# Performance work log

Measured on AMD Instinct MI355X. Metric: run time of the kernel, lower is better.

Reference implementation:

```python
import jax, jax.numpy as jnp
import numpy as np

B, T, C, H = 2, 2048, 1024, 16
D = C // H  # head_dim = 64
CH = C // 2


def _ln(x, g, b, eps=1e-5):
    m = x.mean(-1, keepdims=True)
    v = ((x - m) ** 2).mean(-1, keepdims=True)
    return (x - m) / jnp.sqrt(v + eps) * g + b


def setup_inputs() -> dict:
    key = jax.random.key(0)
    ks = iter(jax.random.split(key, 32))
    w = lambda shp: jax.random.normal(next(ks), shp, dtype=jnp.float32) * 0.02
    inp = {
        'x': jax.random.normal(next(ks), (B, T, C), dtype=jnp.float32),
        'attention_mask': jnp.ones((B, T, T), dtype=jnp.int32),
        # importance_net: Linear(C,C/2), LN(C/2), GELU, Linear(C/2,1), Sigmoid
        'imp_w1': w((C, CH)), 'imp_b1': jnp.zeros((CH,)),
        'imp_g': jnp.ones((CH,)), 'imp_beta': jnp.zeros((CH,)),
        'imp_w2': w((CH, 1)), 'imp_b2': jnp.zeros((1,)),
        # reasoning_net: Linear(C,C), LN(C), GELU, Linear(C,C)
        'rsn_w1': w((C, C)), 'rsn_b1': jnp.zeros((C,)),
        'rsn_g': jnp.ones((C,)), 'rsn_beta': jnp.zeros((C,)),
        'rsn_w2': w((C, C)), 'rsn_b2': jnp.zeros((C,)),
        # attention projections
        'q_w': w((C, C)), 'q_b': jnp.zeros((C,)),
        'k_w': w((C, C)), 'k_b': jnp.zeros((C,)),
        'v_w': w((C, C)), 'v_b': jnp.zeros((C,)),
        'o_w': w((C, C)), 'o_b': jnp.zeros((C,)),
        # temp_net: Linear(C,C/2), LN(C/2), GELU, Linear(C/2,H)
        'tmp_w1': w((C, CH)), 'tmp_b1': jnp.zeros((CH,)),
        'tmp_g': jnp.ones((CH,)), 'tmp_beta': jnp.zeros((CH,)),
        'tmp_w2': w((CH, H)), 'tmp_b2': jnp.zeros((H,)),
        # output LayerNorm
        'norm_g': jnp.ones((C,)), 'norm_b': jnp.zeros((C,)),
    }
    return inp


def reference(x, attention_mask, imp_w1, imp_b1, imp_g, imp_beta, imp_w2, imp_b2,
              rsn_w1, rsn_b1, rsn_g, rsn_beta, rsn_w2, rsn_b2,
              q_w, q_b, k_w, k_b, v_w, v_b, o_w, o_b,
              tmp_w1, tmp_b1, tmp_g, tmp_beta, tmp_w2, tmp_b2,
              norm_g, norm_b):
    Bz, Tz, Cz = x.shape
    # importance gating: [B,T,1]
    h = jax.nn.gelu(_ln(x @ imp_w1 + imp_b1, imp_g, imp_beta), approximate=False)
    importance = jnp.maximum(jax.nn.sigmoid(h @ imp_w2 + imp_b2), 1e-6)
    xi = x * importance
    # reasoning net on gated input
    h = jax.nn.gelu(_ln(xi @ rsn_w1 + rsn_b1, rsn_g, rsn_beta), approximate=False)
    reasoned = h @ rsn_w2 + rsn_b2
    # projections
    q = (reasoned @ q_w + q_b).reshape(Bz, Tz, H, D).transpose(0, 2, 1, 3)
    k = (xi @ k_w + k_b).reshape(Bz, Tz, H, D).transpose(0, 2, 1, 3)
    v = (x @ v_w + v_b).reshape(Bz, Tz, H, D).transpose(0, 2, 1, 3)
    # per-(batch,head) temperature
    ht = jax.nn.gelu(_ln(reasoned.mean(axis=1) @ tmp_w1 + tmp_b1, tmp_g, tmp_beta), approximate=False)
    temp = jax.nn.softplus(ht @ tmp_w2 + tmp_b2) + 0.5  # [B,H]
    # attention with mask and learned temperature before softmax
    scale = 1.0 / jnp.sqrt(jnp.float32(D))
    attn = jnp.einsum('bhqd,bhkd->bhqk', q, k) * scale
    attn = jnp.where(attention_mask[:, None] == 0, -jnp.inf, attn)
    attn = attn * temp[:, :, None, None]
    attn = jax.nn.softmax(attn, axis=-1)
    # dropout is identity in eval mode
    out = jnp.einsum('bhqk,bhkd->bhqd', attn, v)
    out = out.transpose(0, 2, 1, 3).reshape(Bz, Tz, Cz)
    out = out @ o_w + o_b
    return _ln(x + out, norm_g, norm_b)
```

## Files before the change

kernel.cpp:

```cpp
#include <hip/hip_runtime.h>
#include <hip/hip_bf16.h>
#include <math.h>

#define BB 2
#define TT 2048
#define CC 1024
#define HH 16
#define DD 64
#define CHALF 512
#define NN (BB * TT)

typedef __attribute__((ext_vector_type(8))) short short8;
typedef __attribute__((ext_vector_type(4))) short short4_t;
typedef __attribute__((ext_vector_type(4))) float f32x4;

__device__ __forceinline__ float gelu_exact(float x) {
    return 0.5f * x * (1.0f + erff(x * 0.70710678118654752f));
}

__device__ __forceinline__ short f2bf(float f) {
    __hip_bfloat16 h = __float2bfloat16(f);
    short s;
    __builtin_memcpy(&s, &h, 2);
    return s;
}

__device__ __forceinline__ void async_copy16(const void* g, void* l) {
    __builtin_amdgcn_global_load_lds(
        (const __attribute__((address_space(1))) void*)g,
        (__attribute__((address_space(3))) void*)l, 16, 0, 0);
}

__global__ __launch_bounds__(256) void conv_bf16(
    const float* __restrict__ X, __hip_bfloat16* __restrict__ O) {
    int i = (blockIdx.x * 256 + threadIdx.x) * 8;
    float4 a = *(const float4*)&X[i];
    float4 b = *(const float4*)&X[i + 4];
    __hip_bfloat16 o[8] = {
        __float2bfloat16(a.x), __float2bfloat16(a.y),
        __float2bfloat16(a.z), __float2bfloat16(a.w),
        __float2bfloat16(b.x), __float2bfloat16(b.y),
        __float2bfloat16(b.z), __float2bfloat16(b.w)};
    *(float4*)&O[i] = *(float4*)o;
}

__global__ __launch_bounds__(256) void conv_transpose_all(
    const float* w0, const float* w1, const float* w2, const float* w3,
    const float* w4, const float* w5, const float* w6,
    __hip_bfloat16* t0, __hip_bfloat16* t1, __hip_bfloat16* t2,
    __hip_bfloat16* t3, __hip_bfloat16* t4, __hip_bfloat16* t5,
    __hip_bfloat16* t6) {
    const float* W;
    __hip_bfloat16* Wt;
    int N = 1024;
    switch (blockIdx.z) {
        case 0: W = w0; Wt = t0; N = 512; break;
        case 1: W = w1; Wt = t1; break;
        case 2: W = w2; Wt = t2; break;
        case 3: W = w3; Wt = t3; break;
        case 4: W = w4; Wt = t4; break;
        case 5: W = w5; Wt = t5; break;
        default: W = w6; Wt = t6; break;
    }
    int n0 = blockIdx.x * 64, k0 = blockIdx.y * 64;
    if (n0 >= N) return;
    __shared__ float T[64][65];
    int tid = threadIdx.x;
    int c = tid & 63, r4 = tid >> 6;
#pragma unroll
    for (int i = 0; i < 16; ++i) {
        int row = i * 4 + r4;
        T[row][c] = W[(size_t)(k0 + row) * N + n0 + c];
    }
    __syncthreads();
#pragma unroll
    for (int i = 0; i < 16; ++i) {
        int row = i * 4 + r4;
        Wt[(size_t)(n0 + row) * CC + k0 + c] = __float2bfloat16(T[c][row]);
    }
}

template <bool BF16OUT>
__global__ __launch_bounds__(256) void gemm_mfma64(
    const short* __restrict__ A, const short* __restrict__ Wt,
    const float* __restrict__ bias, float* __restrict__ Cf,
    __hip_bfloat16* __restrict__ Cb, int M, int N, int K) {
    __shared__ short As[64][32];
    __shared__ short Bs[128][32];
    int tid = threadIdx.x;
    int wave = tid >> 6, lane = tid & 63;
    int m16 = lane & 15, quad = lane >> 4;
    int wm = wave >> 1, wn = wave & 1;
    int row0 = blockIdx.y * 64, col0 = blockIdx.x * 128;
    int lr = lane >> 2;
    int kof = (lane & 3) * 8;

    f32x4 acc[2][4];
#pragma unroll
    for (int i = 0; i < 2; ++i)
#pragma unroll
        for (int j = 0; j < 4; ++j) acc[i][j] = (f32x4){0.f, 0.f, 0.f, 0.f};

    for (int k0 = 0; k0 < K; k0 += 32) {
        async_copy16(A + (size_t)(row0 + wave * 16 + lr) * K + k0 + kof,
                     &As[wave * 16][0]);
#pragma unroll
        for (int j = 0; j < 2; ++j) {
            int rbase = wave * 32 + j * 16;
            async_copy16(Wt + (size_t)(col0 + rbase + lr) * K + k0 + kof,
                         &Bs[rbase][0]);
        }
        __syncthreads();
        short8 af[2], bfr[4];
#pragma unroll
        for (int i = 0; i < 2; ++i)
            af[i] = *(const short8*)&As[wm * 32 + i * 16 + m16][quad * 8];
#pragma unroll
        for (int j = 0; j < 4; ++j)
            bfr[j] = *(const short8*)&Bs[wn * 64 + j * 16 + m16][quad * 8];
#pragma unroll
        for (int i = 0; i < 2; ++i)
#pragma unroll
            for (int j = 0; j < 4; ++j)
                acc[i][j] = __builtin_amdgcn_mfma_f32_16x16x32_bf16(
                    af[i], bfr[j], acc[i][j], 0, 0, 0);
        __syncthreads();
    }
#pragma unroll
    for (int i = 0; i < 2; ++i) {
#pragma unroll
        for (int j = 0; j < 4; ++j) {
            int col = col0 + wn * 64 + j * 16 + m16;
            float bv = bias[col];
#pragma unroll
            for (int rr = 0; rr < 4; ++rr) {
                int row = row0 + wm * 32 + i * 16 + quad * 4 + rr;
                float val = acc[i][j][rr] + bv;
                if (BF16OUT)
                    Cb[(size_t)row * N + col] = __float2bfloat16(val);
                else
                    Cf[(size_t)row * N + col] = val;
            }
        }
    }
}

__global__ __launch_bounds__(256) void gemm_qkv(
    const short* __restrict__ Aq, const short* __restrict__ Ak,
    const short* __restrict__ Av, const short* __restrict__ Wq,
    const short* __restrict__ Wk, const short* __restrict__ Wv,
    const float* __restrict__ bq, const float* __restrict__ bk,
    const float* __restrict__ bv, __hip_bfloat16* __restrict__ Cq,
    __hip_bfloat16* __restrict__ Ck, __hip_bfloat16* __restrict__ Cv,
    const float* __restrict__ tmp) {
    int z = blockIdx.z;
    const short* A = (z == 0) ? Aq : (z == 1) ? Ak : Av;
    const short* Wt = (z == 0) ? Wq : (z == 1) ? Wk : Wv;
    const float* bias = (z == 0) ? bq : (z == 1) ? bk : bv;
    __hip_bfloat16* C = (z == 0) ? Cq : (z == 1) ? Ck : Cv;

    __shared__ short As[128][32];
    __shared__ short Bs[128][32];
    int tid = threadIdx.x;
    int wave = tid >> 6, lane = tid & 63;
    int m16 = lane & 15, quad = lane >> 4;
    int wm = wave >> 1, wn = wave & 1;
    int row0 = blockIdx.y * 128, col0 = blockIdx.x * 128;
    int lr = lane >> 2;
    int kof = (lane & 3) * 8;

    float scale = 1.0f;
    if (z == 0) scale = tmp[(row0 >> 11) * HH + (col0 >> 6) + wn] * 0.125f;

    f32x4 acc[4][4];
#pragma unroll
    for (int i = 0; i < 4; ++i)
#pragma unroll
        for (int j = 0; j < 4; ++j) acc[i][j] = (f32x4){0.f, 0.f, 0.f, 0.f};

    for (int k0 = 0; k0 < CC; k0 += 32) {
#pragma unroll
        for (int j = 0; j < 2; ++j) {
            int rbase = wave * 32 + j * 16;
            async_copy16(A + (size_t)(row0 + rbase + lr) * CC + k0 + kof,
                         &As[rbase][0]);
            async_copy16(Wt + (size_t)(col0 + rbase + lr) * CC + k0 + kof,
                         &Bs[rbase][0]);
        }
        __syncthreads();
        short8 af[4], bfr[4];
#pragma unroll
        for (int i = 0; i < 4; ++i)
            af[i] = *(const short8*)&As[wm * 64 + i * 16 + m16][quad * 8];
#pragma unroll
        for (int j = 0; j < 4; ++j)
            bfr[j] = *(const short8*)&Bs[wn * 64 + j * 16 + m16][quad * 8];
#pragma unroll
        for (int i = 0; i < 4; ++i)
#pragma unroll
            for (int j = 0; j < 4; ++j)
                acc[i][j] = __builtin_amdgcn_mfma_f32_16x16x32_bf16(
                    af[i], bfr[j], acc[i][j], 0, 0, 0);
        __syncthreads();
    }
#pragma unroll
    for (int i = 0; i < 4; ++i) {
#pragma unroll
        for (int j = 0; j < 4; ++j) {
            int col = col0 + wn * 64 + j * 16 + m16;
            float bv2 = bias[col];
#pragma unroll
            for (int rr = 0; rr < 4; ++rr) {
                int row = row0 + wm * 64 + i * 16 + quad * 4 + rr;
                C[(size_t)row * CC + col] =
                    __float2bfloat16((acc[i][j][rr] + bv2) * scale);
            }
        }
    }
}

template <int WIDTH>
__global__ __launch_bounds__(256) void ln_gelu_kernel(
    float* __restrict__ Y, const float* __restrict__ g,
    const float* __restrict__ beta) {
    constexpr int PT = WIDTH / 256;
    int row = blockIdx.x;
    int tid = threadIdx.x;
    float* yr = Y + (size_t)row * WIDTH;
    float v[PT];
    float s = 0.f;
#pragma unroll
    for (int i = 0; i < PT; ++i) {
        v[i] = yr[i * 256 + tid];
        s += v[i];
    }
    __shared__ float red[256];
    red[tid] = s;
    __syncthreads();
#pragma unroll
    for (int o = 128; o > 0; o >>= 1) {
        if (tid < o) red[tid] += red[tid + o];
        __syncthreads();
    }
    float mean = red[0] * (1.0f / WIDTH);
    __syncthreads();
    s = 0.f;
#pragma unroll
    for (int i = 0; i < PT; ++i) {
        float d = v[i] - mean;
        s += d * d;
    }
    red[tid] = s;
    __syncthreads();
#pragma unroll
    for (int o = 128; o > 0; o >>= 1) {
        if (tid < o) red[tid] += red[tid + o];
        __syncthreads();
    }
    float inv = rsqrtf(red[0] * (1.0f / WIDTH) + 1e-5f);
#pragma unroll
    for (int i = 0; i < PT; ++i) {
        int c = i * 256 + tid;
        yr[c] = gelu_exact((v[i] - mean) * inv * g[c] + beta[c]);
    }
}

template <int WIDTH>
__global__ __launch_bounds__(256) void ln_gelu_bf16(
    const float* __restrict__ Y, const float* __restrict__ g,
    const float* __restrict__ beta, __hip_bfloat16* __restrict__ O) {
    constexpr int PT = WIDTH / 256;
    int row = blockIdx.x;
    int tid = threadIdx.x;
    const float* yr = Y + (size_t)row * WIDTH;
    float v[PT];
    float s = 0.f;
#pragma unroll
    for (int i = 0; i < PT; ++i) {
        v[i] = yr[i * 256 + tid];
        s += v[i];
    }
    __shared__ float red[256];
    red[tid] = s;
    __syncthreads();
#pragma unroll
    for (int o = 128; o > 0; o >>= 1) {
        if (tid < o) red[tid] += red[tid + o];
        __syncthreads();
    }
    float mean = red[0] * (1.0f / WIDTH);
    __syncthreads();
    s = 0.f;
#pragma unroll
    for (int i = 0; i < PT; ++i) {
        float d = v[i] - mean;
        s += d * d;
    }
    red[tid] = s;
    __syncthreads();
#pragma unroll
    for (int o = 128; o > 0; o >>= 1) {
        if (tid < o) red[tid] += red[tid + o];
        __syncthreads();
    }
    float inv = rsqrtf(red[0] * (1.0f / WIDTH) + 1e-5f);
#pragma unroll
    for (int i = 0; i < PT; ++i) {
        int c = i * 256 + tid;
        O[(size_t)row * WIDTH + c] =
            __float2bfloat16(gelu_exact((v[i] - mean) * inv * g[c] + beta[c]));
    }
}

__global__ __launch_bounds__(256) void imp_scale(
    const float* __restrict__ h1, const float* __restrict__ w2,
    const float* __restrict__ b2, const float* __restrict__ x,
    __hip_bfloat16* __restrict__ xi) {
    int row = blockIdx.x;
    int tid = threadIdx.x;
    const float* hr = h1 + (size_t)row * CHALF;
    float s = hr[tid] * w2[tid] + hr[tid + 256] * w2[tid + 256];
    __shared__ float red[256];
    red[tid] = s;
    __syncthreads();
#pragma unroll
    for (int o = 128; o > 0; o >>= 1) {
        if (tid < o) red[tid] += red[tid + o];
        __syncthreads();
    }
    float z = red[0] + b2[0];
    float sg = 1.0f / (1.0f + expf(-z));
    float imp = fmaxf(sg, 1e-6f);
#pragma unroll
    for (int i = 0; i < 4; ++i) {
        int c = i * 256 + tid;
        xi[(size_t)row * CC + c] =
            __float2bfloat16(x[(size_t)row * CC + c] * imp);
    }
}

__global__ __launch_bounds__(256) void mean_part(
    const __hip_bfloat16* __restrict__ R, float* __restrict__ part) {
    int idx = blockIdx.x * 256 + threadIdx.x;
    int c = idx & (CC - 1);
    int chunk = (idx >> 10) & 15;
    int b = idx >> 14;
    const __hip_bfloat16* base = R + ((size_t)(b * TT + chunk * 128)) * CC + c;
    float s = 0.f;
    for (int t = 0; t < 128; ++t) s += __bfloat162float(base[(size_t)t * CC]);
    part[idx] = s;
}

__global__ __launch_bounds__(256) void mean_fin(
    const float* __restrict__ part, float* __restrict__ rm) {
    int idx = blockIdx.x * 256 + threadIdx.x;
    int c = idx & (CC - 1);
    int b = idx >> 10;
    float s = 0.f;
#pragma unroll
    for (int ch = 0; ch < 16; ++ch) s += part[(size_t)(b * 16 + ch) * CC + c];
    rm[idx] = s * (1.0f / TT);
}

__global__ __launch_bounds__(256) void temp_gemv1(
    const float* __restrict__ rm, const float* __restrict__ w1,
    const float* __restrict__ b1, float* __restrict__ acc1) {
    int b = blockIdx.y;
    int c0 = blockIdx.x * 64;
    int tid = threadIdx.x;
    int col = c0 + (tid & 63);
    int kq = tid >> 6;
    const float* rmb = rm + b * CC;
    float s = 0.f;
#pragma unroll 8
    for (int i = kq * 256; i < kq * 256 + 256; ++i)
        s = fmaf(rmb[i], w1[(size_t)i * CHALF + col], s);
    __shared__ float red[256];
    red[tid] = s;
    __syncthreads();
    if (tid < 64) {
        float t = red[tid] + red[tid + 64] + red[tid + 128] + red[tid + 192];
        acc1[b * CHALF + tid + c0] = t + b1[col];
    }
}

__global__ __launch_bounds__(512) void temp_fin(
    const float* __restrict__ acc1, const float* __restrict__ g,
    const float* __restrict__ beta, const float* __restrict__ w2,
    const float* __restrict__ b2, float* __restrict__ temp) {
    __shared__ float red[512];
    __shared__ float wred[8][16];
    int b = blockIdx.x;
    int tid = threadIdx.x;
    int wave = tid >> 6, lane = tid & 63;
    float acc = acc1[b * CHALF + tid];
    red[tid] = acc;
    __syncthreads();
#pragma unroll
    for (int o = 256; o > 0; o >>= 1) {
        if (tid < o) red[tid] += red[tid + o];
        __syncthreads();
    }
    float mean = red[0] * (1.0f / CHALF);
    __syncthreads();
    float d = acc - mean;
    red[tid] = d * d;
    __syncthreads();
#pragma unroll
    for (int o = 256; o > 0; o >>= 1) {
        if (tid < o) red[tid] += red[tid + o];
        __syncthreads();
    }
    float inv = rsqrtf(red[0] * (1.0f / CHALF) + 1e-5f);
    float ht = gelu_exact((acc - mean) * inv * g[tid] + beta[tid]);
    float p[16];
#pragma unroll
    for (int j = 0; j < 16; ++j) p[j] = ht * w2[tid * HH + j];
#pragma unroll
    for (int off = 1; off < 64; off <<= 1)
#pragma unroll
        for (int j = 0; j < 16; ++j) p[j] += __shfl_xor(p[j], off, 64);
    if (lane == 0)
#pragma unroll
        for (int j = 0; j < 16; ++j) wred[wave][j] = p[j];
    __syncthreads();
    if (tid < HH) {
        float s = b2[tid];
#pragma unroll
        for (int w = 0; w < 8; ++w) s += wred[w][tid];
        float sp = fmaxf(s, 0.f) + log1pf(expf(-fabsf(s)));
        temp[b * HH + tid] = sp + 0.5f;
    }
}

__global__ __launch_bounds__(256) void mask_flags(
    const int* __restrict__ mask, int* __restrict__ flags) {
    int kt = blockIdx.x, qt = blockIdx.y, b = blockIdx.z;
    int tid = threadIdx.x;
    int r = tid >> 2;
    int c0 = (tid & 3) * 16;
    const int* base = mask + ((size_t)(b * TT + qt * 64 + r)) * TT + kt * 64 + c0;
    int all = 1;
#pragma unroll
    for (int i = 0; i < 4; ++i) {
        int4 m4 = *(const int4*)(base + i * 4);
        all &= (m4.x != 0) & (m4.y != 0) & (m4.z != 0) & (m4.w != 0);
    }
    __shared__ int red[256];
    red[tid] = all;
    __syncthreads();
#pragma unroll
    for (int o = 128; o > 0; o >>= 1) {
        if (tid < o) red[tid] &= red[tid + o];
        __syncthreads();
    }
    if (tid == 0) flags[(b * 32 + qt) * 32 + kt] = red[0];
}

__global__ __launch_bounds__(256) void transpose_v(
    const short* __restrict__ vb, short* __restrict__ vt) {
    __shared__ short T[64][72];
    int t0 = blockIdx.x * 64;
    int bh = blockIdx.y;
    int b = bh >> 4, h = bh & 15;
    int tid = threadIdx.x;
#pragma unroll
    for (int p = 0; p < 2; ++p) {
        int idx = p * 256 + tid;
        int r = idx >> 3, c = (idx & 7) * 8;
        *(short8*)&T[r][c] =
            *(const short8*)&vb[(size_t)(b * TT + t0 + r) * CC + h * DD + c];
    }
    __syncthreads();
#pragma unroll
    for (int p = 0; p < 2; ++p) {
        int idx = p * 256 + tid;
        int d = idx >> 3, c = (idx & 7) * 8;
        short8 o;
#pragma unroll
        for (int u = 0; u < 8; ++u) o[u] = T[c + u][d];
        *(short8*)&vt[((size_t)bh * DD + d) * TT + t0 + c] = o;
    }
}

__global__ __launch_bounds__(256) void flash_attn_mfma(
    const short* __restrict__ q, const short* __restrict__ k,
    const short* __restrict__ vt, const int* __restrict__ mask,
    const int* __restrict__ flags, __hip_bfloat16* __restrict__ out) {
    __shared__ short Ks[64][72];
    __shared__ short Vt[64][72];
    __shared__ short Ps[128][72];
    int tid = threadIdx.x;
    int wave = tid >> 6, lane = tid & 63;
    int m16 = lane & 15, quad = lane >> 4;
    int qt = blockIdx.x;
    int q0 = qt * 128;
    int bh = blockIdx.y;
    int b = bh >> 4, h = bh & 15;

    short8 qf[2][2];
#pragma unroll
    for (int qg = 0; qg < 2; ++qg) {
        const short* qrow = q + ((size_t)(b * TT + q0 + wave * 32 + qg * 16 + m16)) * CC +
                            h * DD + quad * 8;
        qf[qg][0] = *(const short8*)(qrow);
        qf[qg][1] = *(const short8*)(qrow + 32);
    }

    float m_run[2] = {-INFINITY, -INFINITY};
    float l_run[2] = {0.f, 0.f};
    f32x4 acc_o[2][4];
#pragma unroll
    for (int qg = 0; qg < 2; ++qg)
#pragma unroll
        for (int t = 0; t < 4; ++t) acc_o[qg][t] = (f32x4){0.f, 0.f, 0.f, 0.f};

    for (int kt = 0; kt < TT / 64; ++kt) {
        int kb = kt * 64;
#pragma unroll
        for (int i = 0; i < 2; ++i) {
            int idx = i * 256 + tid;
            int r = idx >> 3;
            int dc = (idx & 7) * 8;
            *(short8*)&Ks[r][dc] =
                *(const short8*)(k + ((size_t)(b * TT + kb + r)) * CC + h * DD + dc);
            *(short8*)&Vt[r][dc] =
                *(const short8*)(vt + ((size_t)bh * DD + r) * TT + kb + dc);
        }
        __syncthreads();

        short8 kf[4][2];
#pragma unroll
        for (int t = 0; t < 4; ++t) {
            kf[t][0] = *(const short8*)&Ks[t * 16 + m16][quad * 8];
            kf[t][1] = *(const short8*)&Ks[t * 16 + m16][32 + quad * 8];
        }
        int fl = flags[(b * 32 + 2 * qt + (wave >> 1)) * 32 + kt];

#pragma unroll
        for (int qg = 0; qg < 2; ++qg) {
            f32x4 sacc[4];
#pragma unroll
            for (int t = 0; t < 4; ++t) sacc[t] = (f32x4){0.f, 0.f, 0.f, 0.f};
#pragma unroll
            for (int t = 0; t < 4; ++t) {
                sacc[t] = __builtin_amdgcn_mfma_f32_16x16x32_bf16(kf[t][0], qf[qg][0], sacc[t], 0, 0, 0);
                sacc[t] = __builtin_amdgcn_mfma_f32_16x16x32_bf16(kf[t][1], qf[qg][1], sacc[t], 0, 0, 0);
            }
            float sv[4][4];
#pragma unroll
            for (int t = 0; t < 4; ++t)
#pragma unroll
                for (int r = 0; r < 4; ++r) sv[t][r] = sacc[t][r];
            if (fl == 0) {
                int qrow = q0 + wave * 32 + qg * 16 + m16;
#pragma unroll
                for (int t = 0; t < 4; ++t)
#pragma unroll
                    for (int r = 0; r < 4; ++r) {
                        int kg = kb + t * 16 + quad * 4 + r;
                        if (mask[((size_t)(b * TT + qrow)) * TT + kg] == 0)
                            sv[t][r] = -INFINITY;
                    }
            }
            float mx = sv[0][0];
#pragma unroll
            for (int t = 0; t < 4; ++t)
#pragma unroll
                for (int r = 0; r < 4; ++r) mx = fmaxf(mx, sv[t][r]);
            mx = fmaxf(mx, __shfl_xor(mx, 16, 64));
            mx = fmaxf(mx, __shfl_xor(mx, 32, 64));
            float mnew = fmaxf(m_run[qg], mx);
            float alpha = __expf(m_run[qg] - mnew);
            m_run[qg] = mnew;
            int prow = wave * 32 + qg * 16 + m16;
            float psum = 0.f;
#pragma unroll
            for (int t = 0; t < 4; ++t) {
                short4_t pk;
#pragma unroll
                for (int r = 0; r < 4; ++r) {
                    float p = __expf(sv[t][r] - mnew);
                    psum += p;
                    pk[r] = f2bf(p);
                }
                *(short4_t*)&Ps[prow][t * 16 + quad * 4] = pk;
            }
            psum += __shfl_xor(psum, 16, 64);
            psum += __shfl_xor(psum, 32, 64);
            l_run[qg] = l_run[qg] * alpha + psum;
#pragma unroll
            for (int r = 0; r < 4; ++r) {
                float ar = __shfl(alpha, (lane & 48) | (quad * 4 + r), 64);
#pragma unroll
                for (int td = 0; td < 4; ++td) acc_o[qg][td][r] *= ar;
            }
        }

#pragma unroll
        for (int kc = 0; kc < 2; ++kc) {
            short8 vf[4];
#pragma unroll
            for (int td = 0; td < 4; ++td)
                vf[td] = *(const short8*)&Vt[td * 16 + m16][kc * 32 + quad * 8];
#pragma unroll
            for (int qg = 0; qg < 2; ++qg) {
                short8 pf = *(const short8*)&Ps[wave * 32 + qg * 16 + m16][kc * 32 + quad * 8];
#pragma unroll
                for (int td = 0; td < 4; ++td)
                    acc_o[qg][td] = __builtin_amdgcn_mfma_f32_16x16x32_bf16(
                        pf, vf[td], acc_o[qg][td], 0, 0, 0);
            }
        }
        __syncthreads();
    }

#pragma unroll
    for (int qg = 0; qg < 2; ++qg) {
#pragma unroll
        for (int r = 0; r < 4; ++r) {
            float lr = __shfl(l_run[qg], (lane & 48) | (quad * 4 + r), 64);
            float inv = 1.0f / lr;
            int row = b * TT + q0 + wave * 32 + qg * 16 + quad * 4 + r;
#pragma unroll
            for (int td = 0; td < 4; ++td)
                out[(size_t)row * CC + h * DD + td * 16 + m16] =
                    __float2bfloat16(acc_o[qg][td][r] * inv);
        }
    }
}

__global__ __launch_bounds__(256) void final_ln(
    const float* __restrict__ x, const float* __restrict__ p,
    const float* __restrict__ g, const float* __restrict__ beta,
    float* __restrict__ out) {
    int row = blockIdx.x;
    int tid = threadIdx.x;
    const float* xr = x + (size_t)row * CC;
    const float* pr = p + (size_t)row * CC;
    float v[4];
    float s = 0.f;
#pragma unroll
    for (int i = 0; i < 4; ++i) {
        int c = i * 256 + tid;
        v[i] = xr[c] + pr[c];
        s += v[i];
    }
    __shared__ float red[256];
    red[tid] = s;
    __syncthreads();
#pragma unroll
    for (int o = 128; o > 0; o >>= 1) {
        if (tid < o) red[tid] += red[tid + o];
        __syncthreads();
    }
    float mean = red[0] * (1.0f / CC);
    __syncthreads();
    s = 0.f;
#pragma unroll
    for (int i = 0; i < 4; ++i) {
        float d = v[i] - mean;
        s += d * d;
    }
    red[tid] = s;
    __syncthreads();
#pragma unroll
    for (int o = 128; o > 0; o >>= 1) {
        if (tid < o) red[tid] += red[tid + o];
        __syncthreads();
    }
    float inv = rsqrtf(red[0] * (1.0f / CC) + 1e-5f);
#pragma unroll
    for (int i = 0; i < 4; ++i) {
        int c = i * 256 + tid;
        out[(size_t)row * CC + c] = (v[i] - mean) * inv * g[c] + beta[c];
    }
}

extern "C" void kernel_launch(void* const* d_in, const int* in_sizes, int n_in,
                              void* d_out, int out_size, void* d_ws,
                              size_t ws_size, hipStream_t stream) {
    const float* x        = (const float*)d_in[0];
    const int*   mask     = (const int*)d_in[1];
    const float* imp_w1   = (const float*)d_in[2];
    const float* imp_b1   = (const float*)d_in[3];
    const float* imp_g    = (const float*)d_in[4];
    const float* imp_beta = (const float*)d_in[5];
    const float* imp_w2   = (const float*)d_in[6];
    const float* imp_b2   = (const float*)d_in[7];
    const float* rsn_w1   = (const float*)d_in[8];
    const float* rsn_b1   = (const float*)d_in[9];
    const float* rsn_g    = (const float*)d_in[10];
    const float* rsn_beta = (const float*)d_in[11];
    const float* rsn_w2   = (const float*)d_in[12];
    const float* rsn_b2   = (const float*)d_in[13];
    const float* q_w      = (const float*)d_in[14];
    const float* q_b      = (const float*)d_in[15];
    const float* k_w      = (const float*)d_in[16];
    const float* k_b      = (const float*)d_in[17];
    const float* v_w      = (const float*)d_in[18];
    const float* v_b      = (const float*)d_in[19];
    const float* o_w      = (const float*)d_in[20];
    const float* o_b      = (const float*)d_in[21];
    const float* tmp_w1   = (const float*)d_in[22];
    const float* tmp_b1   = (const float*)d_in[23];
    const float* tmp_g    = (const float*)d_in[24];
    const float* tmp_beta = (const float*)d_in[25];
    const float* tmp_w2   = (const float*)d_in[26];
    const float* tmp_b2   = (const float*)d_in[27];
    const float* norm_g   = (const float*)d_in[28];
    const float* norm_b   = (const float*)d_in[29];
    float* out = (float*)d_out;
    float* ws  = (float*)d_ws;

    float* h1  = ws;
    float* h2  = ws + 2097152;
    __hip_bfloat16* x_bf  = (__hip_bfloat16*)(ws + 6291456);
    __hip_bfloat16* xi_bf = (__hip_bfloat16*)(ws + 8388608);
    __hip_bfloat16* h2b   = (__hip_bfloat16*)(ws + 10485760);
    __hip_bfloat16* rs_bf = (__hip_bfloat16*)(ws + 12582912);
    __hip_bfloat16* qb    = (__hip_bfloat16*)(ws + 14680064);
    __hip_bfloat16* kb    = (__hip_bfloat16*)(ws + 16777216);
    __hip_bfloat16* vb    = (__hip_bfloat16*)(ws + 18874368);
    __hip_bfloat16* vtb   = (__hip_bfloat16*)(ws + 20971520);
    __hip_bfloat16* imp_w1t = (__hip_bfloat16*)(ws + 23068672);
    __hip_bfloat16* rsn_w1t = (__hip_bfloat16*)(ws + 23330816);
    __hip_bfloat16* rsn_w2t = (__hip_bfloat16*)(ws + 23855104);
    __hip_bfloat16* q_wt    = (__hip_bfloat16*)(ws + 24379392);
    __hip_bfloat16* k_wt    = (__hip_bfloat16*)(ws + 24903680);
    __hip_bfloat16* v_wt    = (__hip_bfloat16*)(ws + 25427968);
    __hip_bfloat16* o_wt    = (__hip_bfloat16*)(ws + 25952256);
    float* rm   = ws + 26476544;
    float* tmp  = ws + 26478592;
    float* part = ws + 26479104;
    int*   flg  = (int*)(ws + 26511872);
    float* acc1 = ws + 26513920;

    dim3 blk(256);
    conv_bf16<<<NN * CC / (256 * 8), blk, 0, stream>>>(x, x_bf);
    conv_transpose_all<<<dim3(16, 16, 7), blk, 0, stream>>>(
        imp_w1, rsn_w1, rsn_w2, q_w, k_w, v_w, o_w,
        imp_w1t, rsn_w1t, rsn_w2t, q_wt, k_wt, v_wt, o_wt);
    mask_flags<<<dim3(32, 32, 2), blk, 0, stream>>>(mask, flg);

    gemm_mfma64<false><<<dim3(CHALF / 128, NN / 64), blk, 0, stream>>>(
        (const short*)x_bf, (const short*)imp_w1t, imp_b1, h1, nullptr, NN, CHALF, CC);
    ln_gelu_kernel<CHALF><<<NN, blk, 0, stream>>>(h1, imp_g, imp_beta);
    imp_scale<<<NN, blk, 0, stream>>>(h1, imp_w2, imp_b2, x, xi_bf);
    gemm_mfma64<false><<<dim3(CC / 128, NN / 64), blk, 0, stream>>>(
        (const short*)xi_bf, (const short*)rsn_w1t, rsn_b1, h2, nullptr, NN, CC, CC);
    ln_gelu_bf16<CC><<<NN, blk, 0, stream>>>(h2, rsn_g, rsn_beta, h2b);
    gemm_mfma64<true><<<dim3(CC / 128, NN / 64), blk, 0, stream>>>(
        (const short*)h2b, (const short*)rsn_w2t, rsn_b2, nullptr, rs_bf, NN, CC, CC);
    mean_part<<<128, blk, 0, stream>>>(rs_bf, part);
    mean_fin<<<8, blk, 0, stream>>>(part, rm);
    temp_gemv1<<<dim3(CHALF / 64, BB), blk, 0, stream>>>(rm, tmp_w1, tmp_b1, acc1);
    temp_fin<<<BB, dim3(512), 0, stream>>>(acc1, tmp_g, tmp_beta, tmp_w2, tmp_b2, tmp);
    gemm_qkv<<<dim3(CC / 128, NN / 128, 3), blk, 0, stream>>>(
        (const short*)rs_bf, (const short*)xi_bf, (const short*)x_bf,
        (const short*)q_wt, (const short*)k_wt, (const short*)v_wt,
        q_b, k_b, v_b, qb, kb, vb, tmp);
    transpose_v<<<dim3(TT / 64, BB * HH), blk, 0, stream>>>(
        (const short*)vb, (short*)vtb);
    flash_attn_mfma<<<dim3(TT / 128, BB * HH), blk, 0, stream>>>(
        (const short*)qb, (const short*)kb, (const short*)vtb, mask, flg, rs_bf);
    gemm_mfma64<false><<<dim3(CC / 128, NN / 64), blk, 0, stream>>>(
        (const short*)rs_bf, (const short*)o_wt, o_b, h2, nullptr, NN, CC, CC);
    final_ln<<<NN, blk, 0, stream>>>(x, h2, norm_g, norm_b, out);
}
```

Before: 444.8 us.

## Merge prep kernels, fuse importance LN/GELU/gate, shrink attention query tile to 64

Three setup kernels (x conversion, weight transposes, mask flags) become one launch, the importance LN+GELU and gating kernels are fused into one, and the mean finalize is folded into temp_gemv1, all to cut launch count and intermediate memory traffic. Flash attention now uses 64-query tiles with one 16-row group per wave, doubling the grid and lowering per-block register use. The Q scale folds in log2(e) so exp2f replaces __expf. The smaller tile gives more blocks but reloads K/V tiles twice as often per query.

```diff
diff --git a/kernel.cpp b/kernel.cpp
--- a/kernel.cpp
+++ b/kernel.cpp
@@ -9,6 +9,7 @@
 #define DD 64
 #define CHALF 512
 #define NN (BB * TT)
+#define LOG2E 1.44269504088896340736f
 
 typedef __attribute__((ext_vector_type(8))) short short8;
 typedef __attribute__((ext_vector_type(4))) short short4_t;
@@ -31,52 +32,86 @@
         (__attribute__((address_space(3))) void*)l, 16, 0, 0);
 }
 
-__global__ __launch_bounds__(256) void conv_bf16(
-    const float* __restrict__ X, __hip_bfloat16* __restrict__ O) {
-    int i = (blockIdx.x * 256 + threadIdx.x) * 8;
-    float4 a = *(const float4*)&X[i];
-    float4 b = *(const float4*)&X[i + 4];
-    __hip_bfloat16 o[8] = {
-        __float2bfloat16(a.x), __float2bfloat16(a.y),
-        __float2bfloat16(a.z), __float2bfloat16(a.w),
-        __float2bfloat16(b.x), __float2bfloat16(b.y),
-        __float2bfloat16(b.z), __float2bfloat16(b.w)};
-    *(float4*)&O[i] = *(float4*)o;
-}
-
-__global__ __launch_bounds__(256) void conv_transpose_all(
+__global__ __launch_bounds__(256) void prep(
+    const float* __restrict__ x, __hip_bfloat16* __restrict__ x_bf,
+    const int* __restrict__ mask, int* __restrict__ flags,
     const float* w0, const float* w1, const float* w2, const float* w3,
     const float* w4, const float* w5, const float* w6,
     __hip_bfloat16* t0, __hip_bfloat16* t1, __hip_bfloat16* t2,
     __hip_bfloat16* t3, __hip_bfloat16* t4, __hip_bfloat16* t5,
     __hip_bfloat16* t6) {
-    const float* W;
-    __hip_bfloat16* Wt;
-    int N = 1024;
-    switch (blockIdx.z) {
-        case 0: W = w0; Wt = t0; N = 512; break;
-        case 1: W = w1; Wt = t1; break;
-        case 2: W = w2; Wt = t2; break;
-        case 3: W = w3; Wt = t3; break;
-        case 4: W = w4; Wt = t4; break;
-        case 5: W = w5; Wt = t5; break;
-        default: W = w6; Wt = t6; break;
-    }
-    int n0 = blockIdx.x * 64, k0 = blockIdx.y * 64;
-    if (n0 >= N) return;
     __shared__ float T[64][65];
-    int tid = threadIdx.x;
-    int c = tid & 63, r4 = tid >> 6;
-#pragma unroll
-    for (int i = 0; i < 16; ++i) {
-        int row = i * 4 + r4;
-        T[row][c] = W[(size_t)(k0 + row) * N + n0 + c];
-    }
-    __syncthreads();
-#pragma unroll
-    for (int i = 0; i < 16; ++i) {
-        int row = i * 4 + r4;
-        Wt[(size_t)(n0 + row) * CC + k0 + c] = __float2bfloat16(T[c][row]);
+    int blk = blockIdx.x;
+    int tid = threadIdx.x;
+    if (blk < 2048) {
+        int i = (blk * 256 + tid) * 8;
+        float4 a = *(const float4*)&x[i];
+        float4 b = *(const float4*)&x[i + 4];
+        __hip_bfloat16 o[8] = {
+            __float2bfloat16(a.x), __float2bfloat16(a.y),
+            __float2bfloat16(a.z), __float2bfloat16(a.w),
+            __float2bfloat16(b.x), __float2bfloat16(b.y),
+            __float2bfloat16(b.z), __float2bfloat16(b.w)};
+        *(float4*)&x_bf[i] = *(float4*)o;
+    } else if (blk < 4096) {
+        int idx = blk - 2048;
+        int kt = idx & 31, qt = (idx >> 5) & 31, b = idx >> 10;
+        int* red = (int*)T;
+        int r = tid >> 2;
+        int c0 = (tid & 3) * 16;
+        const int* base =
+            mask + ((size_t)(b * TT + qt * 64 + r)) * TT + kt * 64 + c0;
+        int all = 1;
+#pragma unroll
+        for (int i = 0; i < 4; ++i) {
+            int4 m4 = *(const int4*)(base + i * 4);
+            all &= (m4.x != 0) & (m4.y != 0) & (m4.z != 0) & (m4.w != 0);
+        }
+        red[tid] = all;
+        __syncthreads();
+#pragma unroll
+        for (int o = 128; o > 0; o >>= 1) {
+            if (tid < o) red[tid] &= red[tid + o];
+            __syncthreads();
+        }
+        if (tid == 0) flags[(b * 32 + qt) * 32 + kt] = red[0];
+    } else {
+        int idx = blk - 4096;
+        const float* W;
+        __hip_bfloat16* Wt;
+        int N, n0, k0;
+        if (idx < 128) {
+            W = w0; Wt = t0; N = 512;
+            n0 = (idx & 7) * 64;
+            k0 = (idx >> 3) * 64;
+        } else {
+            idx -= 128;
+            int w = idx >> 8;
+            int r = idx & 255;
+            N = 1024;
+            n0 = (r & 15) * 64;
+            k0 = (r >> 4) * 64;
+            switch (w) {
+                case 0: W = w1; Wt = t1; break;
+                case 1: W = w2; Wt = t2; break;
+                case 2: W = w3; Wt = t3; break;
+                case 3: W = w4; Wt = t4; break;
+                case 4: W = w5; Wt = t5; break;
+                default: W = w6; Wt = t6; break;
+            }
+        }
+        int c = tid & 63, r4 = tid >> 6;
+#pragma unroll
+        for (int i = 0; i < 16; ++i) {
+            int row = i * 4 + r4;
+            T[row][c] = W[(size_t)(k0 + row) * N + n0 + c];
+        }
+        __syncthreads();
+#pragma unroll
+        for (int i = 0; i < 16; ++i) {
+            int row = i * 4 + r4;
+            Wt[(size_t)(n0 + row) * CC + k0 + c] = __float2bfloat16(T[c][row]);
+        }
     }
 }
 
@@ -170,7 +205,8 @@
     int kof = (lane & 3) * 8;
 
     float scale = 1.0f;
-    if (z == 0) scale = tmp[(row0 >> 11) * HH + (col0 >> 6) + wn] * 0.125f;
+    if (z == 0)
+        scale = tmp[(row0 >> 11) * HH + (col0 >> 6) + wn] * 0.125f * LOG2E;
 
     f32x4 acc[4][4];
 #pragma unroll
@@ -219,49 +255,52 @@
     }
 }
 
-template <int WIDTH>
-__global__ __launch_bounds__(256) void ln_gelu_kernel(
-    float* __restrict__ Y, const float* __restrict__ g,
-    const float* __restrict__ beta) {
-    constexpr int PT = WIDTH / 256;
+__global__ __launch_bounds__(256) void imp_fused(
+    const float* __restrict__ h1, const float* __restrict__ g,
+    const float* __restrict__ beta, const float* __restrict__ w2,
+    const float* __restrict__ b2, const float* __restrict__ x,
+    __hip_bfloat16* __restrict__ xi) {
     int row = blockIdx.x;
     int tid = threadIdx.x;
-    float* yr = Y + (size_t)row * WIDTH;
-    float v[PT];
-    float s = 0.f;
-#pragma unroll
-    for (int i = 0; i < PT; ++i) {
-        v[i] = yr[i * 256 + tid];
-        s += v[i];
-    }
+    const float* hr = h1 + (size_t)row * CHALF;
+    float v0 = hr[tid], v1 = hr[tid + 256];
     __shared__ float red[256];
-    red[tid] = s;
+    red[tid] = v0 + v1;
     __syncthreads();
 #pragma unroll
     for (int o = 128; o > 0; o >>= 1) {
         if (tid < o) red[tid] += red[tid + o];
         __syncthreads();
     }
-    float mean = red[0] * (1.0f / WIDTH);
-    __syncthreads();
-    s = 0.f;
-#pragma unroll
-    for (int i = 0; i < PT; ++i) {
-        float d = v[i] - mean;
-        s += d * d;
-    }
-    red[tid] = s;
+    float mean = red[0] * (1.0f / CHALF);
+    __syncthreads();
+    float d0 = v0 - mean, d1 = v1 - mean;
+    red[tid] = d0 * d0 + d1 * d1;
     __syncthreads();
 #pragma unroll
     for (int o = 128; o > 0; o >>= 1) {
         if (tid < o) red[tid] += red[tid + o];
         __syncthreads();
     }
-    float inv = rsqrtf(red[0] * (1.0f / WIDTH) + 1e-5f);
-#pragma unroll
-    for (int i = 0; i < PT; ++i) {
+    float inv = rsqrtf(red[0] * (1.0f / CHALF) + 1e-5f);
+    __syncthreads();
+    float ge0 = gelu_exact(d0 * inv * g[tid] + beta[tid]);
+    float ge1 = gelu_exact(d1 * inv * g[tid + 256] + beta[tid + 256]);
+    red[tid] = ge0 * w2[tid] + ge1 * w2[tid + 256];
+    __syncthreads();
+#pragma unroll
+    for (int o = 128; o > 0; o >>= 1) {
+        if (tid < o) red[tid] += red[tid + o];
+        __syncthreads();
+    }
+    float z = red[0] + b2[0];
+    float sg = 1.0f / (1.0f + expf(-z));
+    float imp = fmaxf(sg, 1e-6f);
+#pragma unroll
+    for (int i = 0; i < 4; ++i) {
         int c = i * 256 + tid;
-        yr[c] = gelu_exact((v[i] - mean) * inv * g[c] + beta[c]);
+        xi[(size_t)row * CC + c] =
+            __float2bfloat16(x[(size_t)row * CC + c] * imp);
     }
 }
 
@@ -309,33 +348,6 @@
         int c = i * 256 + tid;
         O[(size_t)row * WIDTH + c] =
             __float2bfloat16(gelu_exact((v[i] - mean) * inv * g[c] + beta[c]));
-    }
-}
-
-__global__ __launch_bounds__(256) void imp_scale(
-    const float* __restrict__ h1, const float* __restrict__ w2,
-    const float* __restrict__ b2, const float* __restrict__ x,
-    __hip_bfloat16* __restrict__ xi) {
-    int row = blockIdx.x;
-    int tid = threadIdx.x;
-    const float* hr = h1 + (size_t)row * CHALF;
-    float s = hr[tid] * w2[tid] + hr[tid + 256] * w2[tid + 256];
-    __shared__ float red[256];
-    red[tid] = s;
-    __syncthreads();
-#pragma unroll
-    for (int o = 128; o > 0; o >>= 1) {
-        if (tid < o) red[tid] += red[tid + o];
-        __syncthreads();
-    }
-    float z = red[0] + b2[0];
-    float sg = 1.0f / (1.0f + expf(-z));
-    float imp = fmaxf(sg, 1e-6f);
-#pragma unroll
-    for (int i = 0; i < 4; ++i) {
-        int c = i * 256 + tid;
-        xi[(size_t)row * CC + c] =
-            __float2bfloat16(x[(size_t)row * CC + c] * imp);
     }
 }
 
@@ -351,31 +363,28 @@
     part[idx] = s;
 }
 
-__global__ __launch_bounds__(256) void mean_fin(
-    const float* __restrict__ part, float* __restrict__ rm) {
-    int idx = blockIdx.x * 256 + threadIdx.x;
-    int c = idx & (CC - 1);
-    int b = idx >> 10;
-    float s = 0.f;
-#pragma unroll
-    for (int ch = 0; ch < 16; ++ch) s += part[(size_t)(b * 16 + ch) * CC + c];
-    rm[idx] = s * (1.0f / TT);
-}
-
 __global__ __launch_bounds__(256) void temp_gemv1(
-    const float* __restrict__ rm, const float* __restrict__ w1,
+    const float* __restrict__ part, const float* __restrict__ w1,
     const float* __restrict__ b1, float* __restrict__ acc1) {
+    __shared__ float rm_l[CC];
+    __shared__ float red[256];
     int b = blockIdx.y;
     int c0 = blockIdx.x * 64;
     int tid = threadIdx.x;
+    for (int cc = tid; cc < CC; cc += 256) {
+        float s = 0.f;
+#pragma unroll
+        for (int ch = 0; ch < 16; ++ch)
+            s += part[(size_t)(b * 16 + ch) * CC + cc];
+        rm_l[cc] = s * (1.0f / TT);
+    }
+    __syncthreads();
     int col = c0 + (tid & 63);
     int kq = tid >> 6;
-    const float* rmb = rm + b * CC;
     float s = 0.f;
 #pragma unroll 8
     for (int i = kq * 256; i < kq * 256 + 256; ++i)
-        s = fmaf(rmb[i], w1[(size_t)i * CHALF + col], s);
-    __shared__ float red[256];
+        s = fmaf(rm_l[i], w1[(size_t)i * CHALF + col], s);
     red[tid] = s;
     __syncthreads();
     if (tid < 64) {
@@ -433,30 +442,6 @@
     }
 }
 
-__global__ __launch_bounds__(256) void mask_flags(
-    const int* __restrict__ mask, int* __restrict__ flags) {
-    int kt = blockIdx.x, qt = blockIdx.y, b = blockIdx.z;
-    int tid = threadIdx.x;
-    int r = tid >> 2;
-    int c0 = (tid & 3) * 16;
-    const int* base = mask + ((size_t)(b * TT + qt * 64 + r)) * TT + kt * 64 + c0;
-    int all = 1;
-#pragma unroll
-    for (int i = 0; i < 4; ++i) {
-        int4 m4 = *(const int4*)(base + i * 4);
-        all &= (m4.x != 0) & (m4.y != 0) & (m4.z != 0) & (m4.w != 0);
-    }
-    __shared__ int red[256];
-    red[tid] = all;
-    __syncthreads();
-#pragma unroll
-    for (int o = 128; o > 0; o >>= 1) {
-        if (tid < o) red[tid] &= red[tid + o];
-        __syncthreads();
-    }
-    if (tid == 0) flags[(b * 32 + qt) * 32 + kt] = red[0];
-}
-
 __global__ __launch_bounds__(256) void transpose_v(
     const short* __restrict__ vb, short* __restrict__ vt) {
     __shared__ short T[64][72];
@@ -489,31 +474,24 @@
     const int* __restrict__ flags, __hip_bfloat16* __restrict__ out) {
     __shared__ short Ks[64][72];
     __shared__ short Vt[64][72];
-    __shared__ short Ps[128][72];
+    __shared__ short Ps[64][72];
     int tid = threadIdx.x;
     int wave = tid >> 6, lane = tid & 63;
     int m16 = lane & 15, quad = lane >> 4;
     int qt = blockIdx.x;
-    int q0 = qt * 128;
+    int q0 = qt * 64;
     int bh = blockIdx.y;
     int b = bh >> 4, h = bh & 15;
 
-    short8 qf[2][2];
-#pragma unroll
-    for (int qg = 0; qg < 2; ++qg) {
-        const short* qrow = q + ((size_t)(b * TT + q0 + wave * 32 + qg * 16 + m16)) * CC +
-                            h * DD + quad * 8;
-        qf[qg][0] = *(const short8*)(qrow);
-        qf[qg][1] = *(const short8*)(qrow + 32);
-    }
-
-    float m_run[2] = {-INFINITY, -INFINITY};
-    float l_run[2] = {0.f, 0.f};
-    f32x4 acc_o[2][4];
-#pragma unroll
-    for (int qg = 0; qg < 2; ++qg)
-#pragma unroll
-        for (int t = 0; t < 4; ++t) acc_o[qg][t] = (f32x4){0.f, 0.f, 0.f, 0.f};
+    const short* qrow =
+        q + ((size_t)(b * TT + q0 + wave * 16 + m16)) * CC + h * DD + quad * 8;
+    short8 qf0 = *(const short8*)(qrow);
+    short8 qf1 = *(const short8*)(qrow + 32);
+
+    float m_run = -INFINITY, l_run = 0.f;
+    f32x4 acc_o[4];
+#pragma unroll
+    for (int t = 0; t < 4; ++t) acc_o[t] = (f32x4){0.f, 0.f, 0.f, 0.f};
 
     for (int kt = 0; kt < TT / 64; ++kt) {
         int kb = kt * 64;
@@ -529,104 +507,87 @@
         }
         __syncthreads();
 
-        short8 kf[4][2];
+        f32x4 sacc[4];
+#pragma unroll
+        for (int t = 0; t < 4; ++t) sacc[t] = (f32x4){0.f, 0.f, 0.f, 0.f};
 #pragma unroll
         for (int t = 0; t < 4; ++t) {
-            kf[t][0] = *(const short8*)&Ks[t * 16 + m16][quad * 8];
-            kf[t][1] = *(const short8*)&Ks[t * 16 + m16][32 + quad * 8];
-        }
-        int fl = flags[(b * 32 + 2 * qt + (wave >> 1)) * 32 + kt];
-
-#pragma unroll
-        for (int qg = 0; qg < 2; ++qg) {
-            f32x4 sacc[4];
-#pragma unroll
-            for (int t = 0; t < 4; ++t) sacc[t] = (f32x4){0.f, 0.f, 0.f, 0.f};
-#pragma unroll
-            for (int t = 0; t < 4; ++t) {
-                sacc[t] = __builtin_amdgcn_mfma_f32_16x16x32_bf16(kf[t][0], qf[qg][0], sacc[t], 0, 0, 0);
-                sacc[t] = __builtin_amdgcn_mfma_f32_16x16x32_bf16(kf[t][1], qf[qg][1], sacc[t], 0, 0, 0);
+            short8 kf0 = *(const short8*)&Ks[t * 16 + m16][quad * 8];
+            sacc[t] = __builtin_amdgcn_mfma_f32_16x16x32_bf16(kf0, qf0, sacc[t], 0, 0, 0);
+            short8 kf1 = *(const short8*)&Ks[t * 16 + m16][32 + quad * 8];
+            sacc[t] = __builtin_amdgcn_mfma_f32_16x16x32_bf16(kf1, qf1, sacc[t], 0, 0, 0);
+        }
+        float sv[4][4];
+#pragma unroll
+        for (int t = 0; t < 4; ++t)
+#pragma unroll
+            for (int r = 0; r < 4; ++r) sv[t][r] = sacc[t][r];
+        if (flags[(b * 32 + qt) * 32 + kt] == 0) {
+            int qrg = q0 + wave * 16 + m16;
+#pragma unroll
+            for (int t = 0; t < 4; ++t)
+#pragma unroll
+                for (int r = 0; r < 4; ++r) {
+                    int kg = kb + t * 16 + quad * 4 + r;
+                    if (mask[((size_t)(b * TT + qrg)) * TT + kg] == 0)
+                        sv[t][r] = -INFINITY;
+                }
+        }
+        float mx = sv[0][0];
+#pragma unroll
+        for (int t = 0; t < 4; ++t)
+#pragma unroll
+            for (int r = 0; r < 4; ++r) mx = fmaxf(mx, sv[t][r]);
+        mx = fmaxf(mx, __shfl_xor(mx, 16, 64));
+        mx = fmaxf(mx, __shfl_xor(mx, 32, 64));
+        float mnew = fmaxf(m_run, mx);
+        float alpha = exp2f(m_run - mnew);
+        m_run = mnew;
+        int prow = wave * 16 + m16;
+        float psum = 0.f;
+#pragma unroll
+        for (int t = 0; t < 4; ++t) {
+            short4_t pk;
+#pragma unroll
+            for (int r = 0; r < 4; ++r) {
+                float p = exp2f(sv[t][r] - mnew);
+                psum += p;
+                pk[r] = f2bf(p);
             }
-            float sv[4][4];
-#pragma unroll
-            for (int t = 0; t < 4; ++t)
-#pragma unroll
-                for (int r = 0; r < 4; ++r) sv[t][r] = sacc[t][r];
-            if (fl == 0) {
-                int qrow = q0 + wave * 32 + qg * 16 + m16;
-#pragma unroll
-                for (int t = 0; t < 4; ++t)
-#pragma unroll
-                    for (int r = 0; r < 4; ++r) {
-                        int kg = kb + t * 16 + quad * 4 + r;
-                        if (mask[((size_t)(b * TT + qrow)) * TT + kg] == 0)
-                            sv[t][r] = -INFINITY;
-                    }
+            *(short4_t*)&Ps[prow][t * 16 + quad * 4] = pk;
+        }
+        psum += __shfl_xor(psum, 16, 64);
+        psum += __shfl_xor(psum, 32, 64);
+        l_run = l_run * alpha + psum;
+#pragma unroll
+        for (int r = 0; r < 4; ++r) {
+            float ar = __shfl(alpha, (lane & 48) | (quad * 4 + r), 64);
+#pragma unroll
+            for (int td = 0; td < 4; ++td) acc_o[td][r] *= ar;
+        }
+
+#pragma unroll
+        for (int kc = 0; kc < 2; ++kc) {
+            short8 pf = *(const short8*)&Ps[wave * 16 + m16][kc * 32 + quad * 8];
+#pragma unroll
+            for (int td = 0; td < 4; ++td) {
+                short8 vf = *(const short8*)&Vt[td * 16 + m16][kc * 32 + quad * 8];
+                acc_o[td] = __builtin_amdgcn_mfma_f32_16x16x32_bf16(
+                    pf, vf, acc_o[td], 0, 0, 0);
             }
-            float mx = sv[0][0];
-#pragma unroll
-            for (int t = 0; t < 4; ++t)
-#pragma unroll
-                for (int r = 0; r < 4; ++r) mx = fmaxf(mx, sv[t][r]);
-            mx = fmaxf(mx, __shfl_xor(mx, 16, 64));
-            mx = fmaxf(mx, __shfl_xor(mx, 32, 64));
-            float mnew = fmaxf(m_run[qg], mx);
-            float alpha = __expf(m_run[qg] - mnew);
-            m_run[qg] = mnew;
-            int prow = wave * 32 + qg * 16 + m16;
-            float psum = 0.f;
-#pragma unroll
-            for (int t = 0; t < 4; ++t) {
-                short4_t pk;
-#pragma unroll
-                for (int r = 0; r < 4; ++r) {
-                    float p = __expf(sv[t][r] - mnew);
-                    psum += p;
-                    pk[r] = f2bf(p);
-                }
-                *(short4_t*)&Ps[prow][t * 16 + quad * 4] = pk;
-            }
-            psum += __shfl_xor(psum, 16, 64);
-            psum += __shfl_xor(psum, 32, 64);
-            l_run[qg] = l_run[qg] * alpha + psum;
-#pragma unroll
-            for (int r = 0; r < 4; ++r) {
-                float ar = __shfl(alpha, (lane & 48) | (quad * 4 + r), 64);
-#pragma unroll
-                for (int td = 0; td < 4; ++td) acc_o[qg][td][r] *= ar;
-            }
-        }
-
-#pragma unroll
-        for (int kc = 0; kc < 2; ++kc) {
-            short8 vf[4];
-#pragma unroll
-            for (int td = 0; td < 4; ++td)
-                vf[td] = *(const short8*)&Vt[td * 16 + m16][kc * 32 + quad * 8];
-#pragma unroll
-            for (int qg = 0; qg < 2; ++qg) {
-                short8 pf = *(const short8*)&Ps[wave * 32 + qg * 16 + m16][kc * 32 + quad * 8];
-#pragma unroll
-                for (int td = 0; td < 4; ++td)
-                    acc_o[qg][td] = __builtin_amdgcn_mfma_f32_16x16x32_bf16(
-                        pf, vf[td], acc_o[qg][td], 0, 0, 0);
-            }
-        }
-        __syncthreads();
-    }
-
-#pragma unroll
-    for (int qg = 0; qg < 2; ++qg) {
-#pragma unroll
-        for (int r = 0; r < 4; ++r) {
-            float lr = __shfl(l_run[qg], (lane & 48) | (quad * 4 + r), 64);
-            float inv = 1.0f / lr;
-            int row = b * TT + q0 + wave * 32 + qg * 16 + quad * 4 + r;
-#pragma unroll
-            for (int td = 0; td < 4; ++td)
-                out[(size_t)row * CC + h * DD + td * 16 + m16] =
-                    __float2bfloat16(acc_o[qg][td][r] * inv);
-        }
+        }
+        __syncthreads();
+    }
+
+#pragma unroll
+    for (int r = 0; r < 4; ++r) {
+        float lr = __shfl(l_run, (lane & 48) | (quad * 4 + r), 64);
+        float inv = 1.0f / lr;
+        int row = b * TT + q0 + wave * 16 + quad * 4 + r;
+#pragma unroll
+        for (int td = 0; td < 4; ++td)
+            out[(size_t)row * CC + h * DD + td * 16 + m16] =
+                __float2bfloat16(acc_o[td][r] * inv);
     }
 }
 
@@ -730,31 +691,27 @@
     __hip_bfloat16* k_wt    = (__hip_bfloat16*)(ws + 24903680);
     __hip_bfloat16* v_wt    = (__hip_bfloat16*)(ws + 25427968);
     __hip_bfloat16* o_wt    = (__hip_bfloat16*)(ws + 25952256);
-    float* rm   = ws + 26476544;
     float* tmp  = ws + 26478592;
     float* part = ws + 26479104;
     int*   flg  = (int*)(ws + 26511872);
     float* acc1 = ws + 26513920;
 
     dim3 blk(256);
-    conv_bf16<<<NN * CC / (256 * 8), blk, 0, stream>>>(x, x_bf);
-    conv_transpose_all<<<dim3(16, 16, 7), blk, 0, stream>>>(
+    prep<<<5760, blk, 0, stream>>>(
+        x, x_bf, mask, flg,
         imp_w1, rsn_w1, rsn_w2, q_w, k_w, v_w, o_w,
         imp_w1t, rsn_w1t, rsn_w2t, q_wt, k_wt, v_wt, o_wt);
-    mask_flags<<<dim3(32, 32, 2), blk, 0, stream>>>(mask, flg);
 
     gemm_mfma64<false><<<dim3(CHALF / 128, NN / 64), blk, 0, stream>>>(
         (const short*)x_bf, (const short*)imp_w1t, imp_b1, h1, nullptr, NN, CHALF, CC);
-    ln_gelu_kernel<CHALF><<<NN, blk, 0, stream>>>(h1, imp_g, imp_beta);
-    imp_scale<<<NN, blk, 0, stream>>>(h1, imp_w2, imp_b2, x, xi_bf);
+    imp_fused<<<NN, blk, 0, stream>>>(h1, imp_g, imp_beta, imp_w2, imp_b2, x, xi_bf);
     gemm_mfma64<false><<<dim3(CC / 128, NN / 64), blk, 0, stream>>>(
         (const short*)xi_bf, (const short*)rsn_w1t, rsn_b1, h2, nullptr, NN, CC, CC);
     ln_gelu_bf16<CC><<<NN, blk, 0, stream>>>(h2, rsn_g, rsn_beta, h2b);
     gemm_mfma64<true><<<dim3(CC / 128, NN / 64), blk, 0, stream>>>(
         (const short*)h2b, (const short*)rsn_w2t, rsn_b2, nullptr, rs_bf, NN, CC, CC);
     mean_part<<<128, blk, 0, stream>>>(rs_bf, part);
-    mean_fin<<<8, blk, 0, stream>>>(part, rm);
-    temp_gemv1<<<dim3(CHALF / 64, BB), blk, 0, stream>>>(rm, tmp_w1, tmp_b1, acc1);
+    temp_gemv1<<<dim3(CHALF / 64, BB), blk, 0, stream>>>(part, tmp_w1, tmp_b1, acc1);
     temp_fin<<<BB, dim3(512), 0, stream>>>(acc1, tmp_g, tmp_beta, tmp_w2, tmp_b2, tmp);
     gemm_qkv<<<dim3(CC / 128, NN / 128, 3), blk, 0, stream>>>(
         (const short*)rs_bf, (const short*)xi_bf, (const short*)x_bf,
@@ -762,7 +719,7 @@
         q_b, k_b, v_b, qb, kb, vb, tmp);
     transpose_v<<<dim3(TT / 64, BB * HH), blk, 0, stream>>>(
         (const short*)vb, (short*)vtb);
-    flash_attn_mfma<<<dim3(TT / 128, BB * HH), blk, 0, stream>>>(
+    flash_attn_mfma<<<dim3(TT / 64, BB * HH), blk, 0, stream>>>(
         (const short*)qb, (const short*)kb, (const short*)vtb, mask, flg, rs_bf);
     gemm_mfma64<false><<<dim3(CC / 128, NN / 64), blk, 0, stream>>>(
         (const short*)rs_bf, (const short*)o_wt, o_b, h2, nullptr, NN, CC, CC);
```

After: 443.2 us. About the same (-0.4%).
